# Optimization experiments

Measured on AMD Instinct MI355X. Metric: run time of the kernel, lower is better.

Reference implementation:

```python
import jax, jax.numpy as jnp
import numpy as np

DN = ("NCHW", "OIHW", "NCHW")


def _conv(x, w, b, pad):
    y = jax.lax.conv_general_dilated(x, w, (1, 1), ((pad, pad), (pad, pad)), dimension_numbers=DN)
    return y + b[None, :, None, None]


def _deconv(x, w, b):
    # torch ConvTranspose2d(k=4, s=2, p=1); w: [I, O, 4, 4]
    w_eff = jnp.transpose(w, (1, 0, 2, 3))[:, :, ::-1, ::-1]  # OIHW, rot180
    y = jax.lax.conv_general_dilated(x, w_eff, (1, 1), ((2, 2), (2, 2)), lhs_dilation=(2, 2), dimension_numbers=DN)
    return y + b[None, :, None, None]


def setup_inputs() -> dict:
    key = jax.random.key(0)
    ks = jax.random.split(key, 8)
    C, Cs, H, Hs, K = 256, 768, 256, 8, 2048
    rn = lambda k, shape, scale: jax.random.normal(k, shape, jnp.float32) * scale
    return {
        "down": rn(ks[0], (1, C, H, H), 1.0),
        "swint": rn(ks[1], (1, Cs, Hs, Hs), 1.0),
        "wt_w": rn(ks[2], (C, Cs, 1, 1), 1.0 / np.sqrt(Cs)),
        "wt_b": jnp.zeros((C,), jnp.float32),
        "up_dw": rn(ks[3], (5, C, C, 4, 4), 1.0 / np.sqrt(C * 16)),
        "up_db": jnp.zeros((5, C), jnp.float32),
        "up_cw": rn(ks[4], (5, C, C, 3, 3), 1.0 / np.sqrt(C * 9)),
        "up_cb": jnp.zeros((5, C), jnp.float32),
        "gate_w": rn(ks[5], (1, C, 1, 1), 1.0 / np.sqrt(C)),
        "gate_b": jnp.zeros((1,), jnp.float32),
        "in_w": rn(ks[6], (3 * C, C), 1.0 / np.sqrt(C)),
        "in_b": jnp.zeros((3 * C,), jnp.float32),
        "out_w": rn(ks[7], (C, C), 1.0 / np.sqrt(C)),
        "out_b": jnp.zeros((C,), jnp.float32),
        "k": K,
    }


def reference(down, swint, wt_w, wt_b, up_dw, up_db, up_cw, up_cb, gate_w, gate_b, in_w, in_b, out_w, out_b, k):
    NH = 8
    B, C, H, W = down.shape  # B == 1
    s = _conv(swint, wt_w, wt_b, 0)
    for i in range(up_dw.shape[0]):
        s = _conv(jax.nn.relu(_deconv(s, up_dw[i], up_db[i])), up_cw[i], up_cb[i], 1)
    gate = jax.nn.sigmoid(_conv(down, gate_w, gate_b, 0))  # [1,1,H,W]
    down_flat = down[0].reshape(C, H * W).T  # [HW, C]
    s_flat = s[0].reshape(C, H * W).T        # [HW, C]
    _, idx = jax.lax.top_k(gate.reshape(-1), k)  # [k]
    q_in = down_flat[idx]   # [k, C]
    kv_in = s_flat[idx]     # [k, C]
    # MultiheadAttention (seq-first, batch 1)
    qw, kw, vw = in_w[:C], in_w[C:2 * C], in_w[2 * C:]
    qb, kb, vb = in_b[:C], in_b[C:2 * C], in_b[2 * C:]
    hd = C // NH
    q = (q_in @ qw.T + qb).reshape(k, NH, hd)
    kk = (kv_in @ kw.T + kb).reshape(k, NH, hd)
    v = (kv_in @ vw.T + vb).reshape(k, NH, hd)
    scores = jnp.einsum("qhd,khd->hqk", q, kk) / jnp.sqrt(jnp.asarray(hd, q.dtype))
    attn = jax.nn.softmax(scores, axis=-1)
    o = jnp.einsum("hqk,khd->qhd", attn, v).reshape(k, C)
    o = o @ out_w.T + out_b
    # scatter attended subset back into full feature map
    attended = down_flat.at[idx].set(o)
    return attended.T.reshape(B, C, H, W)
```

## Files before the change

### kernel.cpp

```cpp
#include <hip/hip_runtime.h>
#include <math.h>

#define CCH 256
#define HWP 65536
#define PCI 40

typedef short short8 __attribute__((ext_vector_type(8)));
typedef float f32x4 __attribute__((ext_vector_type(4)));
typedef unsigned short us4 __attribute__((ext_vector_type(4)));

__device__ inline unsigned short f2bf(float f) {
  unsigned u = __float_as_uint(f);
  return (unsigned short)((u + 0x7FFFu + ((u >> 16) & 1u)) >> 16);
}
__device__ inline float bf2f(unsigned short s) {
  return __uint_as_float(((unsigned)s) << 16);
}

__device__ inline void mfma_bf16(f32x4& d, short8 a, short8 b) {
  asm volatile("v_mfma_f32_16x16x32_bf16 %0, %1, %2, %0" : "+v"(d) : "v"(a), "v"(b));
}

static const size_t BUF_B_OFF = 67108864;
static const size_t TAIL_OFF  = 134217728;
static const size_t KEYS_OFF  = TAIL_OFF;
static const size_t HIST_OFF  = TAIL_OFF + 262144;
static const size_t STATE_OFF = TAIL_OFF + 263168;
static const size_t IDX_OFF   = TAIL_OFF + 263424;
static const size_t EQ_OFF    = TAIL_OFF + 271616;
static const size_t OB_OFF    = 6291456;
static const size_t WBI_OFF   = 8388608;
static const size_t WBO_OFF   = 9437184;
static const size_t SROWS_OFF = 10485760;
static const size_t DQ_OFF    = 12582912;
static const size_t GPART_OFF = 16777216;
static const size_t WT5_OFF   = 20971520;
static const size_t QB_OFF    = 31457280;
static const size_t KB_OFF    = 32505856;
static const size_t VT_OFF    = 33554432;
static const size_t CPK_OFF   = 37748736;
static const size_t DPK_OFF   = 44040192;
static const size_t XQ0_OFF   = 57671680;

struct SelState { unsigned int P; int kneed; int nGreater; int nEqual; };

__global__ void k_init(unsigned int* hist, SelState* st) {
  int t = threadIdx.x;
  hist[t] = 0;
  if (t == 0) { st->P = 0u; st->kneed = 2048; st->nGreater = 0; st->nEqual = 0; }
}

__global__ void k_packall(const float* __restrict__ up_cw, const float* __restrict__ up_dw,
                          const float* __restrict__ in_w, const float* __restrict__ out_w,
                          short* __restrict__ cpk, short* __restrict__ dpk,
                          short* __restrict__ wB5, short* __restrict__ wBi,
                          short* __restrict__ wBo) {
  int b = blockIdx.x;
  int tid = threadIdx.x;
  if (b < 1024) {
    int layer = b >> 8, co = b & 255, ci = tid;
    const float* wl = up_cw + (size_t)layer * 589824;
    short* wo = cpk + (size_t)layer * 589824;
    for (int tap = 0; tap < 9; ++tap)
      wo[((size_t)(tap * 256 + co) * 256) + ci] = (short)f2bf(wl[((size_t)(co * 256 + ci)) * 9 + tap]);
  } else if (b < 2304) {
    int bb = b - 1024;
    int layer = bb >> 8, co = bb & 255, ci = tid;
    const float* wl = up_dw + (size_t)layer * 1048576;
    for (int pq = 0; pq < 4; ++pq) {
      int p = pq >> 1, q = pq & 1;
      for (int tt = 0; tt < 4; ++tt) {
        int dyi = tt >> 1, dxi = tt & 1;
        int wr = dyi ? (1 - p) : (3 - p);
        int wc = dxi ? (1 - q) : (3 - q);
        dpk[((size_t)layer * 1048576) + ((size_t)((pq * 4 + tt) * 256 + co) * 256) + ci] =
            (short)f2bf(wl[((size_t)(ci * 256 + co)) * 16 + wr * 4 + wc]);
      }
    }
  } else if (b < 2560) {
    int co = b - 2304;
    const float* w5 = up_cw + 2359296;
    for (int kk = tid; kk < 2304; kk += 256) {
      int c = kk / 288, r = kk % 288;
      int e = r >> 5, cl = r & 31;
      wB5[(size_t)co * 2304 + kk] = (short)f2bf(w5[(size_t)co * 2304 + (size_t)(c * 32 + cl) * 9 + e]);
    }
  } else if (b < 3328) {
    int o = b - 2560;
    wBi[(size_t)o * 256 + tid] = (short)f2bf(in_w[(size_t)o * 256 + tid]);
  } else {
    int o = b - 3328;
    wBo[(size_t)o * 256 + tid] = (short)f2bf(out_w[(size_t)o * 256 + tid]);
  }
}

__global__ __launch_bounds__(256) void k_wtconvM(const float* __restrict__ swint,
                                                 const float* __restrict__ w,
                                                 const float* __restrict__ bias,
                                                 short* __restrict__ xq0) {
  __shared__ short x_s[64 * 40];
  int t = threadIdx.x, l = t & 63, wv = t >> 6;
  int co0 = blockIdx.x * 64;
  f32x4 acc[4];
#pragma unroll
  for (int m = 0; m < 4; ++m) { f32x4 z = {0.f, 0.f, 0.f, 0.f}; acc[m] = z; }
  for (int c0 = 0; c0 < 768; c0 += 32) {
    __syncthreads();
    {
      int ci = t >> 3, pos0 = (t & 7) * 8;
      const float* sp = swint + (size_t)(c0 + ci) * 64 + pos0;
#pragma unroll
      for (int pp = 0; pp < 8; ++pp)
        x_s[(pos0 + pp) * 40 + ci] = (short)f2bf(sp[pp]);
    }
    __syncthreads();
    short8 bfrag = *(const short8*)&x_s[(wv * 16 + (l & 15)) * 40 + (l >> 4) * 8];
#pragma unroll
    for (int m = 0; m < 4; ++m) {
      const float* wp = w + (size_t)(co0 + m * 16 + (l & 15)) * 768 + c0 + (l >> 4) * 8;
      float4 w0 = *(const float4*)wp;
      float4 w1 = *(const float4*)(wp + 4);
      short8 af;
      af[0] = (short)f2bf(w0.x); af[1] = (short)f2bf(w0.y);
      af[2] = (short)f2bf(w0.z); af[3] = (short)f2bf(w0.w);
      af[4] = (short)f2bf(w1.x); af[5] = (short)f2bf(w1.y);
      af[6] = (short)f2bf(w1.z); af[7] = (short)f2bf(w1.w);
      mfma_bf16(acc[m], af, bfrag);
    }
  }
  asm volatile("s_nop 7\n\ts_nop 7" ::);
  int pos = wv * 16 + (l & 15);
#pragma unroll
  for (int m = 0; m < 4; ++m)
#pragma unroll
    for (int r = 0; r < 4; ++r) {
      int co = co0 + m * 16 + (l >> 4) * 4 + r;
      xq0[(size_t)pos * 256 + co] = (short)f2bf(acc[m][r] + bias[co]);
    }
}

__global__ __launch_bounds__(256) void k_deconv8M(const short* __restrict__ xq0,
                                                  const short* __restrict__ wpk,
                                                  const float* __restrict__ bias,
                                                  unsigned* __restrict__ yp) {
  __shared__ short x_s[121 * 260];
  int t = threadIdx.x, l = t & 63, wv = t >> 6;
  int co0 = blockIdx.x * 64;
  int pq = blockIdx.y, p = pq >> 1, q = pq & 1;
  const unsigned* xs32 = (const unsigned*)xq0;
  for (int i = t; i < 121 * 128; i += 256) {
    int row = i >> 7, c2 = i & 127;
    int iy = row / 11 - 1, ix = row % 11 - 1;
    unsigned v = 0;
    if (iy >= 0 && iy < 8 && ix >= 0 && ix < 8)
      v = xs32[(size_t)(iy * 8 + ix) * 128 + c2];
    *(unsigned*)&x_s[row * 260 + 2 * c2] = v;
  }
  __syncthreads();
  f32x4 acc[4];
#pragma unroll
  for (int m = 0; m < 4; ++m) { f32x4 z = {0.f, 0.f, 0.f, 0.f}; acc[m] = z; }
  int pos = wv * 16 + (l & 15);
  int ay = pos >> 3, bx = pos & 7;
#pragma unroll
  for (int tt = 0; tt < 4; ++tt) {
    int dyi = tt >> 1, dxi = tt & 1;
    int rowx = (ay + p + dyi) * 11 + (bx + q + dxi);
#pragma unroll
    for (int c0 = 0; c0 < 256; c0 += 32) {
      short8 bfrag = *(const short8*)&x_s[rowx * 260 + c0 + (l >> 4) * 8];
#pragma unroll
      for (int m = 0; m < 4; ++m) {
        short8 af = *(const short8*)&wpk[((size_t)((pq * 4 + tt) * 256 + co0 + m * 16 + (l & 15)) * 256) + c0 + (l >> 4) * 8];
        mfma_bf16(acc[m], af, bfrag);
      }
    }
  }
  asm volatile("s_nop 7\n\ts_nop 7" ::);
  int oy = 2 * ay + p, ox = 2 * bx + q;
#pragma unroll
  for (int m = 0; m < 4; ++m)
#pragma unroll
    for (int r4p = 0; r4p < 2; ++r4p) {
      int cob = co0 + m * 16 + (l >> 4) * 4 + 2 * r4p;
      unsigned pk = (unsigned)f2bf(fmaxf(acc[m][2 * r4p] + bias[cob], 0.f))
                  | ((unsigned)f2bf(fmaxf(acc[m][2 * r4p + 1] + bias[cob + 1], 0.f)) << 16);
      yp[(size_t)(cob >> 1) * 256 + oy * 16 + ox] = pk;
    }
}

template <int S, int O>
__global__ __launch_bounds__(256) void k_conv3u(const unsigned* __restrict__ xp,
                                                const short* __restrict__ wpk,
                                                const float* __restrict__ bias,
                                                unsigned* __restrict__ yp) {
  constexpr int WPC = (S >= 64) ? 2 : 1;
  constexpr int WCO = 4 / WPC;
  constexpr int COS = 64 / WCO;
  constexpr int MR = COS / 16;
  constexpr int PSP = S / WPC;
  constexpr int NR = PSP / 16;
  constexpr int CBK = (S + 2 + 31) / 32;
  constexpr int RS = O + 2;
  __shared__ short x_s[RS * (S + 2) * PCI];
  unsigned* x_s32 = (unsigned*)x_s;
  int t = threadIdx.x, l = t & 63, wv = t >> 6;
  int wcob = (wv % WCO) * COS;
  int wposb = (wv / WCO) * PSP;
  int row0 = blockIdx.x * O;
  int co0 = blockIdx.y * 64;
  int colb = t & 31, ci2b = t >> 5;
  f32x4 acc[O][MR][NR];
#pragma unroll
  for (int o = 0; o < O; ++o)
#pragma unroll
    for (int m = 0; m < MR; ++m)
#pragma unroll
      for (int n = 0; n < NR; ++n) { f32x4 z = {0.f, 0.f, 0.f, 0.f}; acc[o][m][n] = z; }
  for (int c0 = 0; c0 < CCH; c0 += 32) {
    int cb = c0 >> 1;
    __syncthreads();
#pragma unroll
    for (int r = 0; r < RS; ++r) {
      int gy = row0 - 1 + r;
      bool yok = (gy >= 0 && gy < S);
#pragma unroll
      for (int cbk = 0; cbk < CBK; ++cbk) {
        int col = colb + cbk * 32;
        if (col < S + 2) {
          int gx = col - 1;
          bool ok = yok && (gx >= 0) && (gx < S);
          unsigned v0 = 0, v1 = 0;
          if (ok) {
            size_t gbase = (size_t)(cb + ci2b) * S * S + (size_t)gy * S + gx;
            v0 = xp[gbase];
            v1 = xp[gbase + (size_t)8 * S * S];
          }
          int lb = (r * (S + 2) + col) * (PCI / 2);
          x_s32[lb + ci2b] = v0;
          x_s32[lb + ci2b + 8] = v1;
        }
      }
    }
    __syncthreads();
#pragma unroll
    for (int dyg = 0; dyg < 3; ++dyg)
#pragma unroll
      for (int dx = 0; dx < 3; ++dx) {
        short8 a[MR];
#pragma unroll
        for (int m = 0; m < MR; ++m)
          a[m] = *(const short8*)&wpk[((size_t)((dyg * 3 + dx) * 256 + co0 + wcob + m * 16 + (l & 15)) * 256) + c0 + (l >> 4) * 8];
#pragma unroll
        for (int o = 0; o < O; ++o) {
          short8 b[NR];
#pragma unroll
          for (int n = 0; n < NR; ++n)
            b[n] = *(const short8*)&x_s[((dyg + o) * (S + 2) + wposb + n * 16 + (l & 15) + dx) * PCI + (l >> 4) * 8];
#pragma unroll
          for (int m = 0; m < MR; ++m)
#pragma unroll
            for (int n = 0; n < NR; ++n) mfma_bf16(acc[o][m][n], a[m], b[n]);
        }
      }
  }
  asm volatile("s_nop 7\n\ts_nop 7" ::);
#pragma unroll
  for (int o = 0; o < O; ++o)
#pragma unroll
    for (int m = 0; m < MR; ++m)
#pragma unroll
      for (int n = 0; n < NR; ++n) {
        int cob = co0 + wcob + m * 16 + (l >> 4) * 4;
        int px = wposb + n * 16 + (l & 15);
#pragma unroll
        for (int r4p = 0; r4p < 2; ++r4p) {
          unsigned pk = (unsigned)f2bf(acc[o][m][n][2 * r4p] + bias[cob + 2 * r4p])
                      | ((unsigned)f2bf(acc[o][m][n][2 * r4p + 1] + bias[cob + 2 * r4p + 1]) << 16);
          yp[(size_t)((cob >> 1) + r4p) * S * S + (size_t)(row0 + o) * S + px] = pk;
        }
      }
}

template <int S, int O>
__global__ __launch_bounds__(256) void k_deconvu(const unsigned* __restrict__ xp,
                                                 const short* __restrict__ wpk,
                                                 const float* __restrict__ bias,
                                                 unsigned* __restrict__ yp) {
  constexpr int WPC = (S >= 64) ? 2 : 1;
  constexpr int WCO = 4 / WPC;
  constexpr int COS = 64 / WCO;
  constexpr int MR = COS / 16;
  constexpr int PSP = S / WPC;
  constexpr int NR = PSP / 16;
  constexpr int CBK = (S + 2 + 31) / 32;
  constexpr int RS = O + 1;
  const int SO = 2 * S;
  __shared__ short x_s[RS * (S + 2) * PCI];
  __shared__ short w_s[8 * 64 * PCI];
  unsigned* x_s32 = (unsigned*)x_s;
  int t = threadIdx.x, l = t & 63, wv = t >> 6;
  int wcob = (wv % WCO) * COS;
  int wposb = (wv / WCO) * PSP;
  int row0 = blockIdx.x * O;
  int co0 = blockIdx.y * 64;
  int p = blockIdx.z;
  int colb = t & 31, ci2b = t >> 5;
  f32x4 acc[2][O][MR][NR];
#pragma unroll
  for (int q = 0; q < 2; ++q)
#pragma unroll
    for (int o = 0; o < O; ++o)
#pragma unroll
      for (int m = 0; m < MR; ++m)
#pragma unroll
        for (int n = 0; n < NR; ++n) { f32x4 z = {0.f, 0.f, 0.f, 0.f}; acc[q][o][m][n] = z; }
  for (int c0 = 0; c0 < CCH; c0 += 32) {
    int cb = c0 >> 1;
    __syncthreads();
#pragma unroll
    for (int r = 0; r < RS; ++r) {
      int gy = row0 + p - 1 + r;
      bool yok = (gy >= 0 && gy < S);
#pragma unroll
      for (int cbk = 0; cbk < CBK; ++cbk) {
        int col = colb + cbk * 32;
        if (col < S + 2) {
          int gx = col - 1;
          bool ok = yok && (gx >= 0) && (gx < S);
          unsigned v0 = 0, v1 = 0;
          if (ok) {
            size_t gbase = (size_t)(cb + ci2b) * S * S + (size_t)gy * S + gx;
            v0 = xp[gbase];
            v1 = xp[gbase + (size_t)8 * S * S];
          }
          int lb = (r * (S + 2) + col) * (PCI / 2);
          x_s32[lb + ci2b] = v0;
          x_s32[lb + ci2b + 8] = v1;
        }
      }
    }
    for (int i = t; i < 4096; i += 256) {
      int seg8 = i & 7;
      int rowi = i >> 3;
      int c8 = rowi >> 6, co = rowi & 63;
      int qq = c8 >> 2, tt = c8 & 3;
      us4 wv4 = *(const us4*)&wpk[((size_t)(((2 * p + qq) * 4 + tt) * 256 + co0 + co) * 256) + c0 + seg8 * 4];
      *(us4*)&w_s[rowi * PCI + seg8 * 4] = wv4;
    }
    __syncthreads();
#pragma unroll
    for (int dyi = 0; dyi < 2; ++dyi)
#pragma unroll
      for (int o = 0; o < O; ++o) {
        short8 b[3][NR];
#pragma unroll
        for (int off = 0; off < 3; ++off)
#pragma unroll
          for (int n = 0; n < NR; ++n)
            b[off][n] = *(const short8*)&x_s[((dyi + o) * (S + 2) + wposb + n * 16 + (l & 15) + off) * PCI + (l >> 4) * 8];
#pragma unroll
        for (int q = 0; q < 2; ++q)
#pragma unroll
          for (int dxi = 0; dxi < 2; ++dxi) {
            int c8 = q * 4 + dyi * 2 + dxi;
            short8 a[MR];
#pragma unroll
            for (int m = 0; m < MR; ++m)
              a[m] = *(const short8*)&w_s[(c8 * 64 + wcob + m * 16 + (l & 15)) * PCI + (l >> 4) * 8];
#pragma unroll
            for (int m = 0; m < MR; ++m)
#pragma unroll
              for (int n = 0; n < NR; ++n) mfma_bf16(acc[q][o][m][n], a[m], b[dxi + q][n]);
          }
      }
  }
  asm volatile("s_nop 7\n\ts_nop 7" ::);
#pragma unroll
  for (int o = 0; o < O; ++o) {
    int oy = 2 * (row0 + o) + p;
#pragma unroll
    for (int m = 0; m < MR; ++m)
#pragma unroll
      for (int n = 0; n < NR; ++n) {
        int px = wposb + n * 16 + (l & 15);
#pragma unroll
        for (int r4p = 0; r4p < 2; ++r4p) {
          int cob = co0 + wcob + m * 16 + (l >> 4) * 4 + 2 * r4p;
          float b0 = bias[cob], b1 = bias[cob + 1];
          unsigned pk0 = (unsigned)f2bf(fmaxf(acc[0][o][m][n][2 * r4p] + b0, 0.f))
                       | ((unsigned)f2bf(fmaxf(acc[0][o][m][n][2 * r4p + 1] + b1, 0.f)) << 16);
          unsigned pk1 = (unsigned)f2bf(fmaxf(acc[1][o][m][n][2 * r4p] + b0, 0.f))
                       | ((unsigned)f2bf(fmaxf(acc[1][o][m][n][2 * r4p + 1] + b1, 0.f)) << 16);
          uint2 pk = make_uint2(pk0, pk1);
          *(uint2*)&yp[(size_t)(cob >> 1) * SO * SO + (size_t)oy * SO + 2 * px] = pk;
        }
      }
  }
}

__global__ __launch_bounds__(256) void k_conv3sM(const unsigned* __restrict__ xp,
                                                 const short* __restrict__ wB,
                                                 const float* __restrict__ bias,
                                                 const int* __restrict__ idx,
                                                 short* __restrict__ outb) {
  __shared__ short a_s[16][296];
  __shared__ int py_s[16], px_s[16];
  int t = threadIdx.x, l = t & 63, wv = t >> 6;
  int j0 = blockIdx.x * 16;
  int co0 = blockIdx.y * 128 + wv * 32;
  if (t < 16) {
    int p = idx[j0 + t];
    py_s[t] = p >> 8;
    px_s[t] = p & 255;
  }
  f32x4 acc[2];
  { f32x4 z = {0.f, 0.f, 0.f, 0.f}; acc[0] = z; acc[1] = z; }
  for (int c = 0; c < 8; ++c) {
    __syncthreads();
    for (int i = t; i < 2304; i += 256) {
      int ci2 = i & 15;
      int je = i >> 4;
      int j = je / 9, e = je % 9;
      int gy = py_s[j] - 1 + e / 3, gx = px_s[j] - 1 + e % 3;
      unsigned v = 0;
      if (gy >= 0 && gy < 256 && gx >= 0 && gx < 256)
        v = xp[(size_t)(c * 16 + ci2) * HWP + gy * 256 + gx];
      *(unsigned*)&a_s[j][e * 32 + 2 * ci2] = v;
    }
    __syncthreads();
#pragma unroll
    for (int s = 0; s < 9; ++s) {
      short8 a = *(const short8*)&a_s[l & 15][s * 32 + (l >> 4) * 8];
      int kg = c * 288 + s * 32 + (l >> 4) * 8;
      short8 b0 = *(const short8*)&wB[(size_t)(co0 + (l & 15)) * 2304 + kg];
      short8 b1 = *(const short8*)&wB[(size_t)(co0 + 16 + (l & 15)) * 2304 + kg];
      mfma_bf16(acc[0], a, b0);
      mfma_bf16(acc[1], a, b1);
    }
  }
  asm volatile("s_nop 7\n\ts_nop 7" ::);
#pragma unroll
  for (int n = 0; n < 2; ++n)
#pragma unroll
    for (int r = 0; r < 4; ++r) {
      int j = j0 + (l >> 4) * 4 + r;
      int co = co0 + n * 16 + (l & 15);
      outb[(size_t)j * 256 + co] = (short)f2bf(acc[n][r] + bias[co]);
    }
}

__global__ void k_gatecopy2(const float* __restrict__ down, const float* __restrict__ gw,
                            float* __restrict__ out, float* __restrict__ gpart) {
  int p = blockIdx.x * 256 + threadIdx.x;
  int cc = blockIdx.y;
  float acc = 0.f;
  for (int c = cc * 32; c < cc * 32 + 32; ++c) {
    float v = down[(size_t)c * HWP + p];
    out[(size_t)c * HWP + p] = v;
    acc += v * gw[c];
  }
  gpart[(size_t)cc * HWP + p] = acc;
}

__global__ void k_gkey(const float* __restrict__ gpart, unsigned* __restrict__ keys) {
  int p = blockIdx.x * 256 + threadIdx.x;
  float s = 0.f;
  for (int cc = 0; cc < 8; ++cc) s += gpart[(size_t)cc * HWP + p];
  unsigned u = __float_as_uint(s);
  keys[p] = (u & 0x80000000u) ? ~u : (u | 0x80000000u);
}

__global__ void k_hist(const unsigned int* __restrict__ keys, unsigned int* hist,
                       const SelState* st, int r) {
  __shared__ unsigned int lh[256];
  int t = threadIdx.x;
  lh[t] = 0;
  __syncthreads();
  unsigned int key = keys[blockIdx.x * 256 + t];
  bool ok = (r == 0) || ((key >> (32 - 8 * r)) == st->P);
  if (ok) atomicAdd(&lh[(key >> (24 - 8 * r)) & 255u], 1u);
  __syncthreads();
  if (lh[t]) atomicAdd(&hist[t], lh[t]);
}

__global__ void k_scan(unsigned int* hist, SelState* st) {
  if (threadIdx.x == 0) {
    int need = st->kneed;
    unsigned int cum = 0;
    for (int b = 255; b >= 0; --b) {
      unsigned int h = hist[b];
      if (cum + h >= (unsigned int)need) {
        st->P = (st->P << 8) | (unsigned int)b;
        st->kneed = need - (int)cum;
        break;
      }
      cum += h;
    }
  }
  __syncthreads();
  hist[threadIdx.x] = 0;
}

__global__ void k_compact(const unsigned int* __restrict__ keys, SelState* st,
                          int* __restrict__ idx, int* __restrict__ eq) {
  int p = blockIdx.x * 256 + threadIdx.x;
  unsigned int key = keys[p];
  unsigned int P = st->P;
  if (key > P) {
    int pos = atomicAdd(&st->nGreater, 1);
    idx[pos] = p;
  } else if (key == P) {
    int e = atomicAdd(&st->nEqual, 1);
    if (e < 4096) eq[e] = p;
  }
}

__global__ void k_finalize(SelState* st, int* idx, int* eq) {
  if (threadIdx.x != 0) return;
  int n = st->nEqual;
  if (n > 4096) n = 4096;
  for (int i = 1; i < n; ++i) {
    int v = eq[i], j = i - 1;
    while (j >= 0 && eq[j] > v) { eq[j + 1] = eq[j]; --j; }
    eq[j + 1] = v;
  }
  int g = st->nGreater;
  for (int i = 0; i < st->kneed; ++i) idx[g + i] = eq[i];
}

__global__ void k_gatherq(const float* __restrict__ down, const int* __restrict__ idx,
                          short* __restrict__ dq) {
  int j = blockIdx.x, c = threadIdx.x;
  int p = idx[j];
  dq[(size_t)j * 256 + c] = (short)f2bf(down[(size_t)c * HWP + p]);
}

__global__ __launch_bounds__(256) void k_qkv3(const short* __restrict__ dq,
                                              const short* __restrict__ sr,
                                              const short* __restrict__ wBi,
                                              const float* __restrict__ bias,
                                              short* __restrict__ Qb,
                                              short* __restrict__ Kb,
                                              short* __restrict__ Vt) {
  __shared__ short a_s[16 * 264];
  unsigned* a_s32 = (unsigned*)a_s;
  int t = threadIdx.x, l = t & 63, wv = t >> 6;
  int j0 = blockIdx.x * 16;
  int third = blockIdx.y >> 2;
  const unsigned* s32 = (const unsigned*)(third ? sr : dq);
  for (int i = t; i < 2048; i += 256) {
    int row = i >> 7, c2 = i & 127;
    a_s32[row * 132 + c2] = s32[(size_t)(j0 + row) * 128 + c2];
  }
  __syncthreads();
  int cog = blockIdx.y * 64 + wv * 16 + (l & 15);
  f32x4 acc = {0.f, 0.f, 0.f, 0.f};
  const short* brow = wBi + (size_t)cog * 256 + (l >> 4) * 8;
  const short* arow = a_s + (l & 15) * 264 + (l >> 4) * 8;
#pragma unroll
  for (int kc = 0; kc < 8; ++kc) {
    short8 a = *(const short8*)(arow + kc * 32);
    short8 b = *(const short8*)(brow + kc * 32);
    mfma_bf16(acc, a, b);
  }
  asm volatile("s_nop 7\n\ts_nop 7" ::);
  float bv = bias[cog];
  int co = cog & 255;
  int h = co >> 5, d = co & 31;
#pragma unroll
  for (int r = 0; r < 4; ++r) {
    int j = j0 + (l >> 4) * 4 + r;
    short v = (short)f2bf(acc[r] + bv);
    if (third == 0)      Qb[((size_t)h * 2048 + j) * 32 + d] = v;
    else if (third == 1) Kb[((size_t)h * 2048 + j) * 32 + d] = v;
    else                 Vt[((size_t)h * 32 + d) * 2048 + j] = v;
  }
}

__global__ __launch_bounds__(256) void k_fattn(const short* __restrict__ Qb,
                                               const short* __restrict__ Kb,
                                               const short* __restrict__ Vt,
                                               short* __restrict__ Ob) {
  __shared__ short P_lds[4][16][136];
  int t = threadIdx.x, l = t & 63, wv = t >> 6;
  int h = blockIdx.y;
  int q0 = blockIdx.x * 64 + wv * 16;
  const short* Qh = Qb + (size_t)h * 2048 * 32;
  const short* Kh = Kb + (size_t)h * 2048 * 32;
  const short* Vh = Vt + (size_t)h * 32 * 2048;
  short8 a_q = *(const short8*)&Qh[(size_t)(q0 + (l & 15)) * 32 + (l >> 4) * 8];
  f32x4 o0 = {0.f, 0.f, 0.f, 0.f}, o1 = {0.f, 0.f, 0.f, 0.f};
  float m_run[4], l_run[4];
#pragma unroll
  for (int r = 0; r < 4; ++r) { m_run[r] = -3e38f; l_run[r] = 0.f; }
  const float scale = 0.17677669529663687f;
  for (int k0 = 0; k0 < 2048; k0 += 128) {
    f32x4 s[8];
#pragma unroll
    for (int kt = 0; kt < 8; ++kt) {
      f32x4 z = {0.f, 0.f, 0.f, 0.f};
      s[kt] = z;
      short8 b = *(const short8*)&Kh[(size_t)(k0 + kt * 16 + (l & 15)) * 32 + (l >> 4) * 8];
      mfma_bf16(s[kt], a_q, b);
    }
    asm volatile("s_nop 7\n\ts_nop 7" ::);
    float tm[4];
#pragma unroll
    for (int r = 0; r < 4; ++r) {
      float mx = s[0][r];
#pragma unroll
      for (int kt = 1; kt < 8; ++kt) mx = fmaxf(mx, s[kt][r]);
      tm[r] = mx * scale;
    }
#pragma unroll
    for (int mask = 1; mask < 16; mask <<= 1)
#pragma unroll
      for (int r = 0; r < 4; ++r) tm[r] = fmaxf(tm[r], __shfl_xor(tm[r], mask));
    float mn[4], al[4], rs[4];
#pragma unroll
    for (int r = 0; r < 4; ++r) {
      mn[r] = fmaxf(m_run[r], tm[r]);
      al[r] = __expf(m_run[r] - mn[r]);
      rs[r] = 0.f;
    }
#pragma unroll
    for (int kt = 0; kt < 8; ++kt)
#pragma unroll
      for (int r = 0; r < 4; ++r) {
        float pv = __expf(s[kt][r] * scale - mn[r]);
        s[kt][r] = pv;
        rs[r] += pv;
      }
#pragma unroll
    for (int mask = 1; mask < 16; mask <<= 1)
#pragma unroll
      for (int r = 0; r < 4; ++r) rs[r] += __shfl_xor(rs[r], mask);
#pragma unroll
    for (int r = 0; r < 4; ++r) {
      l_run[r] = l_run[r] * al[r] + rs[r];
      m_run[r] = mn[r];
      o0[r] *= al[r];
      o1[r] *= al[r];
    }
#pragma unroll
    for (int kt = 0; kt < 8; ++kt)
#pragma unroll
      for (int r = 0; r < 4; ++r)
        P_lds[wv][(l >> 4) * 4 + r][kt * 16 + (l & 15)] = (short)f2bf(s[kt][r]);
#pragma unroll
    for (int kc = 0; kc < 4; ++kc) {
      short8 ap = *(const short8*)&P_lds[wv][l & 15][kc * 32 + (l >> 4) * 8];
      short8 b0 = *(const short8*)&Vh[(size_t)(l & 15) * 2048 + k0 + kc * 32 + (l >> 4) * 8];
      short8 b1 = *(const short8*)&Vh[(size_t)(16 + (l & 15)) * 2048 + k0 + kc * 32 + (l >> 4) * 8];
      mfma_bf16(o0, ap, b0);
      mfma_bf16(o1, ap, b1);
    }
  }
  asm volatile("s_nop 7\n\ts_nop 7" ::);
#pragma unroll
  for (int r = 0; r < 4; ++r) {
    float inv = 1.f / l_run[r];
    int qr = q0 + (l >> 4) * 4 + r;
    Ob[(size_t)qr * 256 + h * 32 + (l & 15)] = (short)f2bf(o0[r] * inv);
    Ob[(size_t)qr * 256 + h * 32 + 16 + (l & 15)] = (short)f2bf(o1[r] * inv);
  }
}

__global__ __launch_bounds__(256) void k_outprojM(const short* __restrict__ Ob,
                                                  const short* __restrict__ wBo,
                                                  const float* __restrict__ ob,
                                                  const int* __restrict__ idx,
                                                  float* __restrict__ out) {
  __shared__ short a_s[16 * 264];
  __shared__ int jp[16];
  unsigned* a_s32 = (unsigned*)a_s;
  const unsigned* s32 = (const unsigned*)Ob;
  int t = threadIdx.x, l = t & 63, wv = t >> 6;
  int j0 = blockIdx.x * 16;
  if (t < 16) jp[t] = idx[j0 + t];
  for (int i = t; i < 2048; i += 256) {
    int row = i >> 7, c2 = i & 127;
    a_s32[row * 132 + c2] = s32[(size_t)(j0 + row) * 128 + c2];
  }
  __syncthreads();
  int co = blockIdx.y * 64 + wv * 16 + (l & 15);
  f32x4 acc = {0.f, 0.f, 0.f, 0.f};
  const short* brow = wBo + (size_t)co * 256 + (l >> 4) * 8;
  const short* arow = a_s + (l & 15) * 264 + (l >> 4) * 8;
#pragma unroll
  for (int kc = 0; kc < 8; ++kc) {
    short8 a = *(const short8*)(arow + kc * 32);
    short8 b = *(const short8*)(brow + kc * 32);
    mfma_bf16(acc, a, b);
  }
  asm volatile("s_nop 7\n\ts_nop 7" ::);
  float bv = ob[co];
#pragma unroll
  for (int r = 0; r < 4; ++r) {
    int jl = (l >> 4) * 4 + r;
    out[(size_t)co * HWP + jp[jl]] = acc[r] + bv;
  }
}

extern "C" void kernel_launch(void* const* d_in, const int* in_sizes, int n_in,
                              void* d_out, int out_size, void* d_ws, size_t ws_size,
                              hipStream_t stream) {
  const float* down  = (const float*)d_in[0];
  const float* swint = (const float*)d_in[1];
  const float* wt_w  = (const float*)d_in[2];
  const float* wt_b  = (const float*)d_in[3];
  const float* up_dw = (const float*)d_in[4];
  const float* up_db = (const float*)d_in[5];
  const float* up_cw = (const float*)d_in[6];
  const float* up_cb = (const float*)d_in[7];
  const float* gate_w = (const float*)d_in[8];
  const float* in_w  = (const float*)d_in[10];
  const float* in_b  = (const float*)d_in[11];
  const float* out_w = (const float*)d_in[12];
  const float* out_b = (const float*)d_in[13];
  float* out = (float*)d_out;
  char* ws = (char*)d_ws;

  unsigned* actA = (unsigned*)ws;
  unsigned* actB = (unsigned*)(ws + BUF_B_OFF);
  unsigned int* keys = (unsigned int*)(ws + KEYS_OFF);
  unsigned int* hist = (unsigned int*)(ws + HIST_OFF);
  SelState* st = (SelState*)(ws + STATE_OFF);
  int* idx = (int*)(ws + IDX_OFF);
  int* eq = (int*)(ws + EQ_OFF);
  short* Ob = (short*)(ws + OB_OFF);
  short* wBi = (short*)(ws + WBI_OFF);
  short* wBo = (short*)(ws + WBO_OFF);
  short* srowsb = (short*)(ws + SROWS_OFF);
  short* dq = (short*)(ws + DQ_OFF);
  float* gpart = (float*)(ws + GPART_OFF);
  short* wB5 = (short*)(ws + WT5_OFF);
  short* Qb = (short*)(ws + QB_OFF);
  short* Kb = (short*)(ws + KB_OFF);
  short* Vt = (short*)(ws + VT_OFF);
  short* cpk = (short*)(ws + CPK_OFF);
  short* dpk = (short*)(ws + DPK_OFF);
  short* xq0 = (short*)(ws + XQ0_OFF);

  k_init<<<1, 256, 0, stream>>>(hist, st);

  k_gatecopy2<<<dim3(256, 8), 256, 0, stream>>>(down, gate_w, out, gpart);
  k_gkey<<<256, 256, 0, stream>>>(gpart, keys);
  for (int r = 0; r < 4; ++r) {
    k_hist<<<256, 256, 0, stream>>>(keys, hist, st, r);
    k_scan<<<1, 256, 0, stream>>>(hist, st);
  }
  k_compact<<<256, 256, 0, stream>>>(keys, st, idx, eq);
  k_finalize<<<1, 64, 0, stream>>>(st, idx, eq);

  k_gatherq<<<2048, 256, 0, stream>>>(down, idx, dq);

  k_packall<<<3584, 256, 0, stream>>>(up_cw, up_dw, in_w, out_w, cpk, dpk, wB5, wBi, wBo);

  k_wtconvM<<<4, 256, 0, stream>>>(swint, wt_w, wt_b, xq0);
  k_deconv8M<<<dim3(4, 4), 256, 0, stream>>>(xq0, dpk, up_db, actB);

  k_conv3u<16, 2><<<dim3(8, 4), 256, 0, stream>>>(actB, cpk, up_cb, actA);
  k_deconvu<16, 2><<<dim3(8, 4, 2), 256, 0, stream>>>(actA, dpk + 1048576, up_db + 256, actB);
  k_conv3u<32, 2><<<dim3(16, 4), 256, 0, stream>>>(actB, cpk + 589824, up_cb + 256, actA);
  k_deconvu<32, 2><<<dim3(16, 4, 2), 256, 0, stream>>>(actA, dpk + 2 * 1048576, up_db + 512, actB);
  k_conv3u<64, 1><<<dim3(64, 4), 256, 0, stream>>>(actB, cpk + 2 * 589824, up_cb + 512, actA);
  k_deconvu<64, 1><<<dim3(64, 4, 2), 256, 0, stream>>>(actA, dpk + 3 * 1048576, up_db + 768, actB);
  k_conv3u<128, 1><<<dim3(128, 4), 256, 0, stream>>>(actB, cpk + 3 * 589824, up_cb + 768, actA);
  k_deconvu<128, 2><<<dim3(64, 4, 2), 256, 0, stream>>>(actA, dpk + 4 * 1048576, up_db + 1024, actB);

  k_conv3sM<<<dim3(128, 2), 256, 0, stream>>>(actB, wB5, up_cb + 1024, idx, srowsb);

  k_qkv3<<<dim3(128, 12), 256, 0, stream>>>(dq, srowsb, wBi, in_b, Qb, Kb, Vt);
  k_fattn<<<dim3(32, 8), 256, 0, stream>>>(Qb, Kb, Vt, Ob);
  k_outprojM<<<dim3(128, 4), 256, 0, stream>>>(Ob, wBo, out_b, idx, out);
}
```

Baseline: 699.1 us.

## Fuse top-k radix select and gather into one cooperative grid-synced kernel

```diff
diff --git a/kernel.cpp b/kernel.cpp
--- a/kernel.cpp
+++ b/kernel.cpp
@@ -1,5 +1,8 @@
 #include <hip/hip_runtime.h>
+#include <hip/hip_cooperative_groups.h>
 #include <math.h>
+
+namespace cg = cooperative_groups;
 
 #define CCH 256
 #define HWP 65536
@@ -23,11 +26,10 @@
 
 static const size_t BUF_B_OFF = 67108864;
 static const size_t TAIL_OFF  = 134217728;
-static const size_t KEYS_OFF  = TAIL_OFF;
-static const size_t HIST_OFF  = TAIL_OFF + 262144;
-static const size_t STATE_OFF = TAIL_OFF + 263168;
-static const size_t IDX_OFF   = TAIL_OFF + 263424;
-static const size_t EQ_OFF    = TAIL_OFF + 271616;
+static const size_t HIST4_OFF = TAIL_OFF;
+static const size_t STATE_OFF = TAIL_OFF + 4096;
+static const size_t IDX_OFF   = TAIL_OFF + 8192;
+static const size_t EQ_OFF    = TAIL_OFF + 16384;
 static const size_t OB_OFF    = 6291456;
 static const size_t WBI_OFF   = 8388608;
 static const size_t WBO_OFF   = 9437184;
@@ -43,12 +45,6 @@
 static const size_t XQ0_OFF   = 57671680;
 
 struct SelState { unsigned int P; int kneed; int nGreater; int nEqual; };
-
-__global__ void k_init(unsigned int* hist, SelState* st) {
-  int t = threadIdx.x;
-  hist[t] = 0;
-  if (t == 0) { st->P = 0u; st->kneed = 2048; st->nGreater = 0; st->nEqual = 0; }
-}
 
 __global__ void k_packall(const float* __restrict__ up_cw, const float* __restrict__ up_dw,
                           const float* __restrict__ in_w, const float* __restrict__ out_w,
@@ -94,6 +90,93 @@
   }
 }
 
+__global__ void k_gatecopy2(const float* __restrict__ down, const float* __restrict__ gw,
+                            float* __restrict__ out, float* __restrict__ gpart) {
+  int p = blockIdx.x * 256 + threadIdx.x;
+  int cc = blockIdx.y;
+  float acc = 0.f;
+  for (int c = cc * 32; c < cc * 32 + 32; ++c) {
+    float v = down[(size_t)c * HWP + p];
+    out[(size_t)c * HWP + p] = v;
+    acc += v * gw[c];
+  }
+  gpart[(size_t)cc * HWP + p] = acc;
+}
+
+__global__ void k_topk(const float* __restrict__ gpart,
+                       const float* __restrict__ down,
+                       unsigned* __restrict__ hist4,
+                       SelState* st, int* __restrict__ idx, int* __restrict__ eq,
+                       short* __restrict__ dq) {
+  cg::grid_group grid = cg::this_grid();
+  int b = blockIdx.x, t = threadIdx.x;
+  int p = b * 256 + t;
+  if (b == 0) {
+    for (int i = t; i < 1024; i += 256) hist4[i] = 0;
+    if (t == 0) { st->nGreater = 0; st->nEqual = 0; }
+  }
+  float s = 0.f;
+  for (int cc = 0; cc < 8; ++cc) s += gpart[(size_t)cc * HWP + p];
+  unsigned u = __float_as_uint(s);
+  unsigned key = (u & 0x80000000u) ? ~u : (u | 0x80000000u);
+  grid.sync();
+  unsigned P = 0;
+  int kneed = 2048;
+  __shared__ unsigned lh[256];
+  __shared__ unsigned bcast[2];
+  for (int r = 0; r < 4; ++r) {
+    lh[t] = 0;
+    __syncthreads();
+    bool ok = (r == 0) || ((key >> (32 - 8 * r)) == P);
+    if (ok) atomicAdd(&lh[(key >> (24 - 8 * r)) & 255u], 1u);
+    __syncthreads();
+    if (lh[t]) atomicAdd(&hist4[r * 256 + t], lh[t]);
+    grid.sync();
+    if (t == 0) {
+      unsigned cum = 0, Pn = P;
+      int kn = kneed;
+      for (int bb = 255; bb >= 0; --bb) {
+        unsigned h = hist4[r * 256 + bb];
+        if (cum + h >= (unsigned)kneed) {
+          Pn = (P << 8) | (unsigned)bb;
+          kn = kneed - (int)cum;
+          break;
+        }
+        cum += h;
+      }
+      bcast[0] = Pn;
+      bcast[1] = (unsigned)kn;
+    }
+    __syncthreads();
+    P = bcast[0];
+    kneed = (int)bcast[1];
+  }
+  if (key > P) {
+    int pos = atomicAdd(&st->nGreater, 1);
+    idx[pos] = p;
+  } else if (key == P) {
+    int e = atomicAdd(&st->nEqual, 1);
+    if (e < 4096) eq[e] = p;
+  }
+  grid.sync();
+  if (b == 0 && t == 0) {
+    int n = st->nEqual;
+    if (n > 4096) n = 4096;
+    for (int i = 1; i < n; ++i) {
+      int v = eq[i], j = i - 1;
+      while (j >= 0 && eq[j] > v) { eq[j + 1] = eq[j]; --j; }
+      eq[j + 1] = v;
+    }
+    int g = st->nGreater;
+    for (int i = 0; i < kneed; ++i) idx[g + i] = eq[i];
+  }
+  grid.sync();
+  for (int j = b; j < 2048; j += 256) {
+    int pp = idx[j];
+    dq[(size_t)j * 256 + t] = (short)f2bf(down[(size_t)t * HWP + pp]);
+  }
+}
+
 __global__ __launch_bounds__(256) void k_wtconvM(const float* __restrict__ swint,
                                                  const float* __restrict__ w,
                                                  const float* __restrict__ bias,
@@ -450,92 +533,6 @@
     }
 }
 
-__global__ void k_gatecopy2(const float* __restrict__ down, const float* __restrict__ gw,
-                            float* __restrict__ out, float* __restrict__ gpart) {
-  int p = blockIdx.x * 256 + threadIdx.x;
-  int cc = blockIdx.y;
-  float acc = 0.f;
-  for (int c = cc * 32; c < cc * 32 + 32; ++c) {
-    float v = down[(size_t)c * HWP + p];
-    out[(size_t)c * HWP + p] = v;
-    acc += v * gw[c];
-  }
-  gpart[(size_t)cc * HWP + p] = acc;
-}
-
-__global__ void k_gkey(const float* __restrict__ gpart, unsigned* __restrict__ keys) {
-  int p = blockIdx.x * 256 + threadIdx.x;
-  float s = 0.f;
-  for (int cc = 0; cc < 8; ++cc) s += gpart[(size_t)cc * HWP + p];
-  unsigned u = __float_as_uint(s);
-  keys[p] = (u & 0x80000000u) ? ~u : (u | 0x80000000u);
-}
-
-__global__ void k_hist(const unsigned int* __restrict__ keys, unsigned int* hist,
-                       const SelState* st, int r) {
-  __shared__ unsigned int lh[256];
-  int t = threadIdx.x;
-  lh[t] = 0;
-  __syncthreads();
-  unsigned int key = keys[blockIdx.x * 256 + t];
-  bool ok = (r == 0) || ((key >> (32 - 8 * r)) == st->P);
-  if (ok) atomicAdd(&lh[(key >> (24 - 8 * r)) & 255u], 1u);
-  __syncthreads();
-  if (lh[t]) atomicAdd(&hist[t], lh[t]);
-}
-
-__global__ void k_scan(unsigned int* hist, SelState* st) {
-  if (threadIdx.x == 0) {
-    int need = st->kneed;
-    unsigned int cum = 0;
-    for (int b = 255; b >= 0; --b) {
-      unsigned int h = hist[b];
-      if (cum + h >= (unsigned int)need) {
-        st->P = (st->P << 8) | (unsigned int)b;
-        st->kneed = need - (int)cum;
-        break;
-      }
-      cum += h;
-    }
-  }
-  __syncthreads();
-  hist[threadIdx.x] = 0;
-}
-
-__global__ void k_compact(const unsigned int* __restrict__ keys, SelState* st,
-                          int* __restrict__ idx, int* __restrict__ eq) {
-  int p = blockIdx.x * 256 + threadIdx.x;
-  unsigned int key = keys[p];
-  unsigned int P = st->P;
-  if (key > P) {
-    int pos = atomicAdd(&st->nGreater, 1);
-    idx[pos] = p;
-  } else if (key == P) {
-    int e = atomicAdd(&st->nEqual, 1);
-    if (e < 4096) eq[e] = p;
-  }
-}
-
-__global__ void k_finalize(SelState* st, int* idx, int* eq) {
-  if (threadIdx.x != 0) return;
-  int n = st->nEqual;
-  if (n > 4096) n = 4096;
-  for (int i = 1; i < n; ++i) {
-    int v = eq[i], j = i - 1;
-    while (j >= 0 && eq[j] > v) { eq[j + 1] = eq[j]; --j; }
-    eq[j + 1] = v;
-  }
-  int g = st->nGreater;
-  for (int i = 0; i < st->kneed; ++i) idx[g + i] = eq[i];
-}
-
-__global__ void k_gatherq(const float* __restrict__ down, const int* __restrict__ idx,
-                          short* __restrict__ dq) {
-  int j = blockIdx.x, c = threadIdx.x;
-  int p = idx[j];
-  dq[(size_t)j * 256 + c] = (short)f2bf(down[(size_t)c * HWP + p]);
-}
-
 __global__ __launch_bounds__(256) void k_qkv3(const short* __restrict__ dq,
                                               const short* __restrict__ sr,
                                               const short* __restrict__ wBi,
@@ -724,8 +721,7 @@
 
   unsigned* actA = (unsigned*)ws;
   unsigned* actB = (unsigned*)(ws + BUF_B_OFF);
-  unsigned int* keys = (unsigned int*)(ws + KEYS_OFF);
-  unsigned int* hist = (unsigned int*)(ws + HIST_OFF);
+  unsigned* hist4 = (unsigned*)(ws + HIST4_OFF);
   SelState* st = (SelState*)(ws + STATE_OFF);
   int* idx = (int*)(ws + IDX_OFF);
   int* eq = (int*)(ws + EQ_OFF);
@@ -743,18 +739,15 @@
   short* dpk = (short*)(ws + DPK_OFF);
   short* xq0 = (short*)(ws + XQ0_OFF);
 
-  k_init<<<1, 256, 0, stream>>>(hist, st);
-
   k_gatecopy2<<<dim3(256, 8), 256, 0, stream>>>(down, gate_w, out, gpart);
-  k_gkey<<<256, 256, 0, stream>>>(gpart, keys);
-  for (int r = 0; r < 4; ++r) {
-    k_hist<<<256, 256, 0, stream>>>(keys, hist, st, r);
-    k_scan<<<1, 256, 0, stream>>>(hist, st);
-  }
-  k_compact<<<256, 256, 0, stream>>>(keys, st, idx, eq);
-  k_finalize<<<1, 64, 0, stream>>>(st, idx, eq);
-
-  k_gatherq<<<2048, 256, 0, stream>>>(down, idx, dq);
+
+  {
+    const float* gp = gpart;
+    const float* dn = down;
+    void* args[] = {(void*)&gp, (void*)&dn, (void*)&hist4, (void*)&st,
+                    (void*)&idx, (void*)&eq, (void*)&dq};
+    hipLaunchCooperativeKernel((void*)k_topk, dim3(256), dim3(256), args, 0, stream);
+  }
 
   k_packall<<<3584, 256, 0, stream>>>(up_cw, up_dw, in_w, out_w, cpk, dpk, wB5, wBi, wBo);
 
```

Measured after the change: 855.2 us. +22.3%, slower.
